# Kernel tuning notes

Hardware: AMD Instinct MI355X
Metric: run time of the kernel (lower is better)

Reference implementation:

```python
import jax, jax.numpy as jnp
import numpy as np

B, PTS, D = 8, 4096, 256          # batch, points per sample, hidden_size
QT, QR, QO = 3000, 216, 1         # num_queries: pos bins, 72*3 euler bins, openness


def setup_inputs() -> dict:
    key = jax.random.key(0)
    ks = jax.random.split(key, 11)
    N = B * PTS
    w = lambda k, s: jax.random.normal(k, s, jnp.float32) * 0.02
    return {
        "feat": jax.random.normal(ks[0], (N, D), jnp.float32),
        "npoints_in_batch": jnp.full((B,), PTS, jnp.int32),
        "queries_t": w(ks[1], (QT, D)),
        "Wk_t": w(ks[2], (D, D)),
        "Wv_t": w(ks[3], (D, D)),
        "queries_r": w(ks[4], (QR, D)),
        "Wk_r": w(ks[5], (D, D)),
        "Wv_r": w(ks[6], (D, D)),
        "queries_o": w(ks[7], (QO, D)),
        "Wk_o": w(ks[8], (D, D)),
        "Wv_o": w(ks[9], (D, D)),
    }


def _aggregate(feat, seg, queries, Wk, Wv):
    """Ragged cross-attention pooling + sum over feature dim.

    feat: (N, D) all points; seg: (N,) sample id per point.
    Equivalent to, per sample b: sum_d( softmax_n(q K_b^T/sqrt(D)) V_b )[q, d]
    => (B, Q) since sum over d commutes: attn @ V.sum(-1).
    """
    d = feat.shape[-1]
    k = feat @ Wk                                  # (N, D)
    vsum = (feat @ Wv).sum(-1)                     # (N,)  row-sum of values
    scores = (k @ queries.T) / jnp.sqrt(jnp.float32(d))  # (N, Q)
    m = jax.ops.segment_max(scores, seg, num_segments=B)  # (B, Q)
    e = jnp.exp(scores - m[seg])                   # (N, Q)
    denom = jax.ops.segment_sum(e, seg, num_segments=B)   # (B, Q)
    numer = jax.ops.segment_sum(e * vsum[:, None], seg, num_segments=B)
    return numer / denom                           # (B, Q)


def reference(feat, npoints_in_batch, queries_t, Wk_t, Wv_t,
              queries_r, Wk_r, Wv_r, queries_o, Wk_o, Wv_o):
    N = feat.shape[0]
    seg = jnp.repeat(jnp.arange(B, dtype=jnp.int32), npoints_in_batch,
                     total_repeat_length=N)
    xt = _aggregate(feat, seg, queries_t, Wk_t, Wv_t)  # (B, 3000)
    xr = _aggregate(feat, seg, queries_r, Wk_r, Wv_r)  # (B, 216)
    xo = _aggregate(feat, seg, queries_o, Wk_o, Wv_o)  # (B, 1)
    return (xt, xr, xo)
```

## Files before the change

kernel.cpp:

```cpp
#include <hip/hip_runtime.h>

typedef __attribute__((ext_vector_type(8))) short short8;
typedef __attribute__((ext_vector_type(4))) float f32x4;
typedef unsigned int u32;

#define D_ 256
#define QT_V 3000
#define QR_V 216
#define QO_V 1
#define QPT 3008
#define QPR 224
#define QPO 96
#define QPTOT 3328
#define WQ_TILES 104
#define NSPLIT 8
#define VPAD 32
#define SCALE 0.09016844005556021f
#define TILE_US 8192
#define PSTRIDE 264

__device__ __forceinline__ unsigned short f2bf(float f) {
    union { float f; unsigned int i; } u; u.f = f;
    unsigned int i = u.i + 0x7fffu + ((u.i >> 16) & 1u);
    return (unsigned short)(i >> 16);
}

__device__ __forceinline__ void async_cp16(const unsigned short* g, unsigned short* l) {
    __builtin_amdgcn_global_load_lds((const __attribute__((address_space(1))) u32*)g,
                                     (__attribute__((address_space(3))) u32*)l, 16, 0, 0);
}

__global__ __launch_bounds__(256) void prep_small(
    const float* __restrict__ wk_t, const float* __restrict__ wk_r,
    const float* __restrict__ wk_o,
    const float* __restrict__ wv_t, const float* __restrict__ wv_r,
    const float* __restrict__ wv_o,
    unsigned short* __restrict__ Wkb,
    float* __restrict__ wvsum, float* __restrict__ vsum, int N)
{
    int blk = blockIdx.x, tid = (int)threadIdx.x;
    if (blk < 3) {
        const float* Wk = (blk == 0) ? wk_t : ((blk == 1) ? wk_r : wk_o);
        const float* Wv = (blk == 0) ? wv_t : ((blk == 1) ? wv_r : wv_o);
        for (int i = tid; i < 16384; i += 256) {
            float4 v = ((const float4*)Wk)[i];
            ushort4 o;
            o.x = f2bf(v.x); o.y = f2bf(v.y); o.z = f2bf(v.z); o.w = f2bf(v.w);
            ((ushort4*)(Wkb + (size_t)blk * 65536))[i] = o;
        }
        const float* row = Wv + (size_t)tid * D_;
        float s = 0.f;
        for (int d = 0; d < D_; d += 4) {
            float4 v = *(const float4*)(row + d);
            s += v.x + v.y + v.z + v.w;
        }
        wvsum[blk * 256 + tid] = s;
    } else {
        if (tid < 3 * VPAD) {
            int h = tid / VPAD, i = tid % VPAD;
            vsum[(size_t)h * (N + VPAD) + N + i] = 0.f;
        }
    }
}

__global__ __launch_bounds__(256) void prep_mid(
    const float* __restrict__ feat,
    const float* __restrict__ wvsum,
    const float* __restrict__ q_t, const float* __restrict__ q_r,
    const float* __restrict__ q_o,
    const unsigned short* __restrict__ Wkb,
    unsigned short* __restrict__ featb,
    float* __restrict__ vsum,
    unsigned short* __restrict__ WqT,
    int N, int ntiles)
{
    __shared__ __align__(16) unsigned short lds[32 * PSTRIDE];
    int blk = blockIdx.x, tid = (int)threadIdx.x;
    int srow = tid >> 3, c8 = tid & 7;
    int wave = tid >> 6, lane = tid & 63;
    int col16 = lane & 15, quad = lane >> 4;

    if (blk < ntiles) {
        int t = blk;
        int row = t * 32 + srow;
        bool valid = row < N;
        float p0 = 0.f, p1 = 0.f, p2 = 0.f;
#pragma unroll
        for (int i = 0; i < 8; ++i) {
            int col = i * 32 + c8 * 4;
            float4 v;
            if (valid) v = *(const float4*)(feat + (size_t)row * D_ + col);
            else { v.x = v.y = v.z = v.w = 0.f; }
            ushort4 o;
            o.x = f2bf(v.x); o.y = f2bf(v.y); o.z = f2bf(v.z); o.w = f2bf(v.w);
            *(ushort4*)(lds + srow * PSTRIDE + col) = o;
            float4 w0 = *(const float4*)(wvsum + col);
            float4 w1 = *(const float4*)(wvsum + 256 + col);
            float4 w2 = *(const float4*)(wvsum + 512 + col);
            p0 += v.x * w0.x + v.y * w0.y + v.z * w0.z + v.w * w0.w;
            p1 += v.x * w1.x + v.y * w1.y + v.z * w1.z + v.w * w1.w;
            p2 += v.x * w2.x + v.y * w2.y + v.z * w2.z + v.w * w2.w;
        }
        p0 += __shfl_xor(p0, 1); p0 += __shfl_xor(p0, 2); p0 += __shfl_xor(p0, 4);
        p1 += __shfl_xor(p1, 1); p1 += __shfl_xor(p1, 2); p1 += __shfl_xor(p1, 4);
        p2 += __shfl_xor(p2, 1); p2 += __shfl_xor(p2, 2); p2 += __shfl_xor(p2, 4);
        if (c8 == 0 && valid) {
            vsum[0 * (size_t)(N + VPAD) + row] = p0;
            vsum[1 * (size_t)(N + VPAD) + row] = p1;
            vsum[2 * (size_t)(N + VPAD) + row] = p2;
        }
        __syncthreads();
#pragma unroll
        for (int i = 0; i < 4; ++i) {
            int cmb = wave * 4 + i;
            int kk = cmb >> 1, sub = cmb & 1;
            short8 v = *(const short8*)(lds + (sub * 16 + col16) * PSTRIDE
                                        + quad * 8 + kk * 32);
            *(short8*)(featb + (size_t)t * TILE_US + cmb * 512 + lane * 8) = v;
        }
    } else {
        int wq = blk - ntiles;
        const float* Q; int nvalid, lq0, outrow, h;
        if (wq < 94)       { Q = q_t; nvalid = QT_V; lq0 = wq * 32;         outrow = lq0;             h = 0; }
        else if (wq < 101) { Q = q_r; nvalid = QR_V; lq0 = (wq - 94) * 32;  outrow = QPT + lq0;       h = 1; }
        else               { Q = q_o; nvalid = QO_V; lq0 = (wq - 101) * 32; outrow = QPT + QPR + lq0; h = 2; }
        int row = lq0 + srow;
        bool valid = row < nvalid;
#pragma unroll
        for (int i = 0; i < 8; ++i) {
            int col = i * 32 + c8 * 4;
            float4 v;
            if (valid) v = *(const float4*)(Q + (size_t)row * D_ + col);
            else { v.x = v.y = v.z = v.w = 0.f; }
            ushort4 o;
            o.x = f2bf(v.x); o.y = f2bf(v.y); o.z = f2bf(v.z); o.w = f2bf(v.w);
            *(ushort4*)(lds + srow * PSTRIDE + col) = o;
        }
        __syncthreads();
        int c0 = wave * 64;
        f32x4 acc[2][4];
#pragma unroll
        for (int mt = 0; mt < 2; ++mt)
#pragma unroll
            for (int nt = 0; nt < 4; ++nt)
                acc[mt][nt] = f32x4{0.f, 0.f, 0.f, 0.f};
        const unsigned short* Wh = Wkb + (size_t)h * 65536;
#pragma unroll
        for (int kk = 0; kk < 8; ++kk) {
            short8 a0 = *(const short8*)(lds + col16 * PSTRIDE + quad * 8 + kk * 32);
            short8 a1 = *(const short8*)(lds + (16 + col16) * PSTRIDE + quad * 8 + kk * 32);
#pragma unroll
            for (int nt = 0; nt < 4; ++nt) {
                short8 bf = *(const short8*)(Wh + (size_t)(c0 + nt * 16 + col16) * D_
                                             + quad * 8 + kk * 32);
                acc[0][nt] = __builtin_amdgcn_mfma_f32_16x16x32_bf16(a0, bf, acc[0][nt], 0, 0, 0);
                acc[1][nt] = __builtin_amdgcn_mfma_f32_16x16x32_bf16(a1, bf, acc[1][nt], 0, 0, 0);
            }
        }
#pragma unroll
        for (int mt = 0; mt < 2; ++mt)
#pragma unroll
            for (int nt = 0; nt < 4; ++nt)
#pragma unroll
                for (int r = 0; r < 4; ++r) {
                    int orow = outrow + mt * 16 + quad * 4 + r;
                    int ocol = c0 + nt * 16 + col16;
                    WqT[(size_t)orow * D_ + ocol] = f2bf(acc[mt][nt][r] * SCALE);
                }
    }
}

__global__ __launch_bounds__(256, 4) void attn_main(
    const unsigned short* __restrict__ featb,
    const int* __restrict__ npts,
    const unsigned short* __restrict__ WqT,
    const float* __restrict__ vsum,
    float* __restrict__ partials, int N)
{
    __shared__ __align__(16) unsigned short lds[2][TILE_US];
    int b = blockIdx.z, qblock = blockIdx.y, chunk = blockIdx.x;
    int tid = (int)threadIdx.x;
    int wave = tid >> 6, lane = tid & 63;
    int col = lane & 15, quad = lane >> 4;

    int qp0 = qblock * 128 + wave * 32;
    int h = (qp0 < QPT) ? 0 : ((qp0 < QPT + QPR) ? 1 : 2);
    const float* vs = vsum + (size_t)h * (N + VPAD);

    int start = 0;
#pragma unroll 1
    for (int i = 0; i < b; ++i) start += npts[i];
    int end = start + npts[b];
    if (end > N) end = N;
    if (start < 0) start = 0;
    if (start > end) start = end;
    int bt0 = start >> 5, bt1 = (end + 31) >> 5;
    int ntc = (bt1 - bt0 + NSPLIT - 1) / NSPLIT;
    int ta = bt0 + chunk * ntc;
    int tb = ta + ntc; if (tb > bt1) tb = bt1;

    short8 bfrag[2][8];
#pragma unroll
    for (int qt = 0; qt < 2; ++qt) {
        const unsigned short* wr = WqT + (size_t)(qp0 + qt * 16 + col) * D_ + quad * 8;
#pragma unroll
        for (int kk = 0; kk < 8; ++kk)
            bfrag[qt][kk] = *(const short8*)(wr + kk * 32);
    }

    float den0 = 0.f, num0 = 0.f, den1 = 0.f, num1 = 0.f;
    int p = 0;
    if (ta < tb) {
        const unsigned short* g = featb + (size_t)ta * TILE_US + (wave * 4) * 512 + lane * 8;
#pragma unroll
        for (int i = 0; i < 4; ++i)
            async_cp16(g + i * 512, &lds[0][(wave * 4 + i) * 512]);
    }
#pragma unroll 1
    for (int t = ta; t < tb; ++t) {
        __syncthreads();
        if (t + 1 < tb) {
            const unsigned short* g = featb + (size_t)(t + 1) * TILE_US + (wave * 4) * 512 + lane * 8;
#pragma unroll
            for (int i = 0; i < 4; ++i)
                async_cp16(g + i * 512, &lds[p ^ 1][(wave * 4 + i) * 512]);
        }
        const unsigned short* lp = lds[p];
        f32x4 acc00 = {0.f,0.f,0.f,0.f}, acc01 = {0.f,0.f,0.f,0.f};
        f32x4 acc10 = {0.f,0.f,0.f,0.f}, acc11 = {0.f,0.f,0.f,0.f};
#pragma unroll
        for (int kk = 0; kk < 8; ++kk) {
            short8 a0 = *(const short8*)(lp + (kk * 2 + 0) * 512 + lane * 8);
            short8 a1 = *(const short8*)(lp + (kk * 2 + 1) * 512 + lane * 8);
            acc00 = __builtin_amdgcn_mfma_f32_16x16x32_bf16(a0, bfrag[0][kk], acc00, 0, 0, 0);
            acc10 = __builtin_amdgcn_mfma_f32_16x16x32_bf16(a0, bfrag[1][kk], acc10, 0, 0, 0);
            acc01 = __builtin_amdgcn_mfma_f32_16x16x32_bf16(a1, bfrag[0][kk], acc01, 0, 0, 0);
            acc11 = __builtin_amdgcn_mfma_f32_16x16x32_bf16(a1, bfrag[1][kk], acc11, 0, 0, 0);
        }
        int rb = t * 32 + quad * 4;
        f32x4 v0 = *(const f32x4*)(vs + rb);
        f32x4 v1 = *(const f32x4*)(vs + rb + 16);
        int r0 = t * 32;
        if (r0 >= start && r0 + 32 <= end) {
#pragma unroll
            for (int r = 0; r < 4; ++r) {
                float e00 = __builtin_amdgcn_exp2f(acc00[r]);
                float e01 = __builtin_amdgcn_exp2f(acc01[r]);
                float e10 = __builtin_amdgcn_exp2f(acc10[r]);
                float e11 = __builtin_amdgcn_exp2f(acc11[r]);
                den0 += e00 + e01; num0 += e00 * v0[r] + e01 * v1[r];
                den1 += e10 + e11; num1 += e10 * v0[r] + e11 * v1[r];
            }
        } else {
#pragma unroll
            for (int r = 0; r < 4; ++r) {
                int ra = rb + r, rb2 = rb + 16 + r;
                bool ma = (ra >= start) && (ra < end);
                bool mb = (rb2 >= start) && (rb2 < end);
                float e00 = ma ? __builtin_amdgcn_exp2f(acc00[r]) : 0.f;
                float e01 = mb ? __builtin_amdgcn_exp2f(acc01[r]) : 0.f;
                float e10 = ma ? __builtin_amdgcn_exp2f(acc10[r]) : 0.f;
                float e11 = mb ? __builtin_amdgcn_exp2f(acc11[r]) : 0.f;
                den0 += e00 + e01; num0 += e00 * v0[r] + e01 * v1[r];
                den1 += e10 + e11; num1 += e10 * v0[r] + e11 * v1[r];
            }
        }
        p ^= 1;
    }

    den0 += __shfl_xor(den0, 16); den0 += __shfl_xor(den0, 32);
    num0 += __shfl_xor(num0, 16); num0 += __shfl_xor(num0, 32);
    den1 += __shfl_xor(den1, 16); den1 += __shfl_xor(den1, 32);
    num1 += __shfl_xor(num1, 16); num1 += __shfl_xor(num1, 32);

    if (quad == 0) {
        size_t base = ((size_t)b * QPTOT + (qp0 + col)) * NSPLIT + chunk;
        partials[base * 2]     = den0;
        partials[base * 2 + 1] = num0;
        size_t base1 = base + (size_t)16 * NSPLIT;
        partials[base1 * 2]     = den1;
        partials[base1 * 2 + 1] = num1;
    }
}

__global__ __launch_bounds__(256) void combine_k(
    const float* __restrict__ partials,
    float* __restrict__ out, int Bn)
{
    int gid = blockIdx.x * 256 + threadIdx.x;
    int total = Bn * QPTOT;
    if (gid >= total) return;
    int b = gid / QPTOT, qp = gid - b * QPTOT;
    const float* p = partials + (size_t)gid * NSPLIT * 2;
    float den = 0.f, num = 0.f;
#pragma unroll
    for (int c = 0; c < NSPLIT; ++c) { den += p[c * 2]; num += p[c * 2 + 1]; }
    float val = (den > 0.f) ? (num / den) : 0.f;
    int oidx = -1;
    if (qp < QPT) {
        if (qp < QT_V) oidx = b * QT_V + qp;
    } else if (qp < QPT + QPR) {
        int q = qp - QPT;
        if (q < QR_V) oidx = Bn * QT_V + b * QR_V + q;
    } else {
        int q = qp - QPT - QPR;
        if (q < QO_V) oidx = Bn * (QT_V + QR_V) + b;
    }
    if (oidx >= 0) out[oidx] = val;
}

extern "C" void kernel_launch(void* const* d_in, const int* in_sizes, int n_in,
                              void* d_out, int out_size, void* d_ws, size_t ws_size,
                              hipStream_t stream)
{
    const float* feat = (const float*)d_in[0];
    const int* npts   = (const int*)d_in[1];
    const float* q_t  = (const float*)d_in[2];
    const float* wk_t = (const float*)d_in[3];
    const float* wv_t = (const float*)d_in[4];
    const float* q_r  = (const float*)d_in[5];
    const float* wk_r = (const float*)d_in[6];
    const float* wv_r = (const float*)d_in[7];
    const float* q_o  = (const float*)d_in[8];
    const float* wk_o = (const float*)d_in[9];
    const float* wv_o = (const float*)d_in[10];

    int N  = in_sizes[0] / D_;
    int Bn = in_sizes[1];
    int ntiles = (N + 31) / 32;

    char* ws = (char*)d_ws;
    size_t off = 0;
    unsigned short* WqT = (unsigned short*)(ws + off);
    off += (size_t)QPTOT * D_ * sizeof(unsigned short);
    off = (off + 255) & ~(size_t)255;
    unsigned short* featb = (unsigned short*)(ws + off);
    off += (size_t)ntiles * TILE_US * sizeof(unsigned short);
    off = (off + 255) & ~(size_t)255;
    unsigned short* Wkb = (unsigned short*)(ws + off);
    off += (size_t)3 * 65536 * sizeof(unsigned short);
    off = (off + 255) & ~(size_t)255;
    float* wvsum = (float*)(ws + off);
    off += 3 * D_ * sizeof(float);
    off = (off + 255) & ~(size_t)255;
    float* vsum = (float*)(ws + off);
    off += (size_t)3 * (N + VPAD) * sizeof(float);
    off = (off + 255) & ~(size_t)255;
    float* partials = (float*)(ws + off);
    off += (size_t)Bn * QPTOT * NSPLIT * 2 * sizeof(float);
    (void)ws_size;

    prep_small<<<4, 256, 0, stream>>>(wk_t, wk_r, wk_o, wv_t, wv_r, wv_o,
                                      Wkb, wvsum, vsum, N);
    prep_mid<<<ntiles + WQ_TILES, 256, 0, stream>>>(feat, wvsum, q_t, q_r, q_o,
                                                    Wkb, featb, vsum, WqT, N, ntiles);

    dim3 grid(NSPLIT, QPTOT / 128, Bn);
    attn_main<<<grid, 256, 0, stream>>>(featb, npts, WqT, vsum, partials, N);

    int total = Bn * QPTOT;
    combine_k<<<(total + 255) / 256, 256, 0, stream>>>(partials, (float*)d_out, Bn);
}
```

Before: 189.8 us.

## Load feature tiles directly from global into registers instead of LDS double-buffer

Removes the LDS double-buffered async global-to-LDS pipeline and the per-tile block barrier in attn_main. Each wave now loads its MFMA A-fragments for a tile straight from global memory into registers and then issues the MFMAs. The change also splits the softmax accumulators into independent per-fragment partial sums and lowers the launch-bounds occupancy hint from 4 to 3 blocks per CU to allow more registers. The aim is to drop barrier and LDS overhead. In exchange, every wave in a block re-reads the same tile from global memory or cache, and load latency is no longer hidden by explicit prefetching.

```diff
diff --git a/kernel.cpp b/kernel.cpp
--- a/kernel.cpp
+++ b/kernel.cpp
@@ -25,11 +25,6 @@
     return (unsigned short)(i >> 16);
 }
 
-__device__ __forceinline__ void async_cp16(const unsigned short* g, unsigned short* l) {
-    __builtin_amdgcn_global_load_lds((const __attribute__((address_space(1))) u32*)g,
-                                     (__attribute__((address_space(3))) u32*)l, 16, 0, 0);
-}
-
 __global__ __launch_bounds__(256) void prep_small(
     const float* __restrict__ wk_t, const float* __restrict__ wk_r,
     const float* __restrict__ wk_o,
@@ -170,14 +165,13 @@
     }
 }
 
-__global__ __launch_bounds__(256, 4) void attn_main(
+__global__ __launch_bounds__(256, 3) void attn_main(
     const unsigned short* __restrict__ featb,
     const int* __restrict__ npts,
     const unsigned short* __restrict__ WqT,
     const float* __restrict__ vsum,
     float* __restrict__ partials, int N)
 {
-    __shared__ __align__(16) unsigned short lds[2][TILE_US];
     int b = blockIdx.z, qblock = blockIdx.y, chunk = blockIdx.x;
     int tid = (int)threadIdx.x;
     int wave = tid >> 6, lane = tid & 63;
@@ -208,38 +202,31 @@
             bfrag[qt][kk] = *(const short8*)(wr + kk * 32);
     }
 
-    float den0 = 0.f, num0 = 0.f, den1 = 0.f, num1 = 0.f;
-    int p = 0;
-    if (ta < tb) {
-        const unsigned short* g = featb + (size_t)ta * TILE_US + (wave * 4) * 512 + lane * 8;
-#pragma unroll
-        for (int i = 0; i < 4; ++i)
-            async_cp16(g + i * 512, &lds[0][(wave * 4 + i) * 512]);
-    }
+    float den00 = 0.f, den01 = 0.f, den10 = 0.f, den11 = 0.f;
+    float num00 = 0.f, num01 = 0.f, num10 = 0.f, num11 = 0.f;
+
 #pragma unroll 1
     for (int t = ta; t < tb; ++t) {
-        __syncthreads();
-        if (t + 1 < tb) {
-            const unsigned short* g = featb + (size_t)(t + 1) * TILE_US + (wave * 4) * 512 + lane * 8;
-#pragma unroll
-            for (int i = 0; i < 4; ++i)
-                async_cp16(g + i * 512, &lds[p ^ 1][(wave * 4 + i) * 512]);
-        }
-        const unsigned short* lp = lds[p];
-        f32x4 acc00 = {0.f,0.f,0.f,0.f}, acc01 = {0.f,0.f,0.f,0.f};
-        f32x4 acc10 = {0.f,0.f,0.f,0.f}, acc11 = {0.f,0.f,0.f,0.f};
-#pragma unroll
-        for (int kk = 0; kk < 8; ++kk) {
-            short8 a0 = *(const short8*)(lp + (kk * 2 + 0) * 512 + lane * 8);
-            short8 a1 = *(const short8*)(lp + (kk * 2 + 1) * 512 + lane * 8);
-            acc00 = __builtin_amdgcn_mfma_f32_16x16x32_bf16(a0, bfrag[0][kk], acc00, 0, 0, 0);
-            acc10 = __builtin_amdgcn_mfma_f32_16x16x32_bf16(a0, bfrag[1][kk], acc10, 0, 0, 0);
-            acc01 = __builtin_amdgcn_mfma_f32_16x16x32_bf16(a1, bfrag[0][kk], acc01, 0, 0, 0);
-            acc11 = __builtin_amdgcn_mfma_f32_16x16x32_bf16(a1, bfrag[1][kk], acc11, 0, 0, 0);
-        }
+        const unsigned short* tp = featb + (size_t)t * TILE_US + lane * 8;
         int rb = t * 32 + quad * 4;
         f32x4 v0 = *(const f32x4*)(vs + rb);
         f32x4 v1 = *(const f32x4*)(vs + rb + 16);
+
+        short8 a0[8], a1[8];
+#pragma unroll
+        for (int kk = 0; kk < 8; ++kk) {
+            a0[kk] = *(const short8*)(tp + (kk * 2 + 0) * 512);
+            a1[kk] = *(const short8*)(tp + (kk * 2 + 1) * 512);
+        }
+        f32x4 acc00 = {0.f,0.f,0.f,0.f}, acc01 = {0.f,0.f,0.f,0.f};
+        f32x4 acc10 = {0.f,0.f,0.f,0.f}, acc11 = {0.f,0.f,0.f,0.f};
+#pragma unroll
+        for (int kk = 0; kk < 8; ++kk) {
+            acc00 = __builtin_amdgcn_mfma_f32_16x16x32_bf16(a0[kk], bfrag[0][kk], acc00, 0, 0, 0);
+            acc10 = __builtin_amdgcn_mfma_f32_16x16x32_bf16(a0[kk], bfrag[1][kk], acc10, 0, 0, 0);
+            acc01 = __builtin_amdgcn_mfma_f32_16x16x32_bf16(a1[kk], bfrag[0][kk], acc01, 0, 0, 0);
+            acc11 = __builtin_amdgcn_mfma_f32_16x16x32_bf16(a1[kk], bfrag[1][kk], acc11, 0, 0, 0);
+        }
         int r0 = t * 32;
         if (r0 >= start && r0 + 32 <= end) {
 #pragma unroll
@@ -248,8 +235,10 @@
                 float e01 = __builtin_amdgcn_exp2f(acc01[r]);
                 float e10 = __builtin_amdgcn_exp2f(acc10[r]);
                 float e11 = __builtin_amdgcn_exp2f(acc11[r]);
-                den0 += e00 + e01; num0 += e00 * v0[r] + e01 * v1[r];
-                den1 += e10 + e11; num1 += e10 * v0[r] + e11 * v1[r];
+                den00 += e00; num00 += e00 * v0[r];
+                den01 += e01; num01 += e01 * v1[r];
+                den10 += e10; num10 += e10 * v0[r];
+                den11 += e11; num11 += e11 * v1[r];
             }
         } else {
 #pragma unroll
@@ -261,13 +250,16 @@
                 float e01 = mb ? __builtin_amdgcn_exp2f(acc01[r]) : 0.f;
                 float e10 = ma ? __builtin_amdgcn_exp2f(acc10[r]) : 0.f;
                 float e11 = mb ? __builtin_amdgcn_exp2f(acc11[r]) : 0.f;
-                den0 += e00 + e01; num0 += e00 * v0[r] + e01 * v1[r];
-                den1 += e10 + e11; num1 += e10 * v0[r] + e11 * v1[r];
+                den00 += e00; num00 += e00 * v0[r];
+                den01 += e01; num01 += e01 * v1[r];
+                den10 += e10; num10 += e10 * v0[r];
+                den11 += e11; num11 += e11 * v1[r];
             }
         }
-        p ^= 1;
-    }
-
+    }
+
+    float den0 = den00 + den01, num0 = num00 + num01;
+    float den1 = den10 + den11, num1 = num10 + num11;
     den0 += __shfl_xor(den0, 16); den0 += __shfl_xor(den0, 32);
     num0 += __shfl_xor(num0, 16); num0 += __shfl_xor(num0, 32);
     den1 += __shfl_xor(den1, 16); den1 += __shfl_xor(den1, 32);
```

New measurement: 230.6 us. 1.22x slower.

## Merge prep kernels into one launch and raise split count of attention

Applied to the files above, without the earlier changes.

Folds the small weight-prep kernel into a single prep launch. The Wk bf16 conversion now happens inline, with fp32 weights read directly inside the WqT MFMA loop. Wv row-sums and the vsum projection move into a separate set of blocks that each recompute the Wv sums. This removes one kernel launch and a serial dependency. NSPLIT doubles from 8 to 16 to give the attention kernel more blocks across the point dimension, at the cost of more partials for the combine step to reduce.

```diff
diff --git a/kernel.cpp b/kernel.cpp
--- a/kernel.cpp
+++ b/kernel.cpp
@@ -13,7 +13,7 @@
 #define QPO 96
 #define QPTOT 3328
 #define WQ_TILES 104
-#define NSPLIT 8
+#define NSPLIT 16
 #define VPAD 32
 #define SCALE 0.09016844005556021f
 #define TILE_US 8192
@@ -30,49 +30,18 @@
                                      (__attribute__((address_space(3))) u32*)l, 16, 0, 0);
 }
 
-__global__ __launch_bounds__(256) void prep_small(
+__global__ __launch_bounds__(256) void prep(
+    const float* __restrict__ feat,
+    const float* __restrict__ q_t, const float* __restrict__ q_r,
+    const float* __restrict__ q_o,
     const float* __restrict__ wk_t, const float* __restrict__ wk_r,
     const float* __restrict__ wk_o,
     const float* __restrict__ wv_t, const float* __restrict__ wv_r,
     const float* __restrict__ wv_o,
-    unsigned short* __restrict__ Wkb,
-    float* __restrict__ wvsum, float* __restrict__ vsum, int N)
-{
-    int blk = blockIdx.x, tid = (int)threadIdx.x;
-    if (blk < 3) {
-        const float* Wk = (blk == 0) ? wk_t : ((blk == 1) ? wk_r : wk_o);
-        const float* Wv = (blk == 0) ? wv_t : ((blk == 1) ? wv_r : wv_o);
-        for (int i = tid; i < 16384; i += 256) {
-            float4 v = ((const float4*)Wk)[i];
-            ushort4 o;
-            o.x = f2bf(v.x); o.y = f2bf(v.y); o.z = f2bf(v.z); o.w = f2bf(v.w);
-            ((ushort4*)(Wkb + (size_t)blk * 65536))[i] = o;
-        }
-        const float* row = Wv + (size_t)tid * D_;
-        float s = 0.f;
-        for (int d = 0; d < D_; d += 4) {
-            float4 v = *(const float4*)(row + d);
-            s += v.x + v.y + v.z + v.w;
-        }
-        wvsum[blk * 256 + tid] = s;
-    } else {
-        if (tid < 3 * VPAD) {
-            int h = tid / VPAD, i = tid % VPAD;
-            vsum[(size_t)h * (N + VPAD) + N + i] = 0.f;
-        }
-    }
-}
-
-__global__ __launch_bounds__(256) void prep_mid(
-    const float* __restrict__ feat,
-    const float* __restrict__ wvsum,
-    const float* __restrict__ q_t, const float* __restrict__ q_r,
-    const float* __restrict__ q_o,
-    const unsigned short* __restrict__ Wkb,
     unsigned short* __restrict__ featb,
+    unsigned short* __restrict__ WqT,
     float* __restrict__ vsum,
-    unsigned short* __restrict__ WqT,
-    int N, int ntiles)
+    int N, int ntiles, int nvs)
 {
     __shared__ __align__(16) unsigned short lds[32 * PSTRIDE];
     int blk = blockIdx.x, tid = (int)threadIdx.x;
@@ -84,7 +53,6 @@
         int t = blk;
         int row = t * 32 + srow;
         bool valid = row < N;
-        float p0 = 0.f, p1 = 0.f, p2 = 0.f;
 #pragma unroll
         for (int i = 0; i < 8; ++i) {
             int col = i * 32 + c8 * 4;
@@ -94,20 +62,6 @@
             ushort4 o;
             o.x = f2bf(v.x); o.y = f2bf(v.y); o.z = f2bf(v.z); o.w = f2bf(v.w);
             *(ushort4*)(lds + srow * PSTRIDE + col) = o;
-            float4 w0 = *(const float4*)(wvsum + col);
-            float4 w1 = *(const float4*)(wvsum + 256 + col);
-            float4 w2 = *(const float4*)(wvsum + 512 + col);
-            p0 += v.x * w0.x + v.y * w0.y + v.z * w0.z + v.w * w0.w;
-            p1 += v.x * w1.x + v.y * w1.y + v.z * w1.z + v.w * w1.w;
-            p2 += v.x * w2.x + v.y * w2.y + v.z * w2.z + v.w * w2.w;
-        }
-        p0 += __shfl_xor(p0, 1); p0 += __shfl_xor(p0, 2); p0 += __shfl_xor(p0, 4);
-        p1 += __shfl_xor(p1, 1); p1 += __shfl_xor(p1, 2); p1 += __shfl_xor(p1, 4);
-        p2 += __shfl_xor(p2, 1); p2 += __shfl_xor(p2, 2); p2 += __shfl_xor(p2, 4);
-        if (c8 == 0 && valid) {
-            vsum[0 * (size_t)(N + VPAD) + row] = p0;
-            vsum[1 * (size_t)(N + VPAD) + row] = p1;
-            vsum[2 * (size_t)(N + VPAD) + row] = p2;
         }
         __syncthreads();
 #pragma unroll
@@ -118,12 +72,12 @@
                                         + quad * 8 + kk * 32);
             *(short8*)(featb + (size_t)t * TILE_US + cmb * 512 + lane * 8) = v;
         }
-    } else {
+    } else if (blk < ntiles + WQ_TILES) {
         int wq = blk - ntiles;
-        const float* Q; int nvalid, lq0, outrow, h;
-        if (wq < 94)       { Q = q_t; nvalid = QT_V; lq0 = wq * 32;         outrow = lq0;             h = 0; }
-        else if (wq < 101) { Q = q_r; nvalid = QR_V; lq0 = (wq - 94) * 32;  outrow = QPT + lq0;       h = 1; }
-        else               { Q = q_o; nvalid = QO_V; lq0 = (wq - 101) * 32; outrow = QPT + QPR + lq0; h = 2; }
+        const float* Q; const float* Wh; int nvalid, lq0, outrow;
+        if (wq < 94)       { Q = q_t; Wh = wk_t; nvalid = QT_V; lq0 = wq * 32;         outrow = lq0; }
+        else if (wq < 101) { Q = q_r; Wh = wk_r; nvalid = QR_V; lq0 = (wq - 94) * 32;  outrow = QPT + lq0; }
+        else               { Q = q_o; Wh = wk_o; nvalid = QO_V; lq0 = (wq - 101) * 32; outrow = QPT + QPR + lq0; }
         int row = lq0 + srow;
         bool valid = row < nvalid;
 #pragma unroll
@@ -144,15 +98,20 @@
 #pragma unroll
             for (int nt = 0; nt < 4; ++nt)
                 acc[mt][nt] = f32x4{0.f, 0.f, 0.f, 0.f};
-        const unsigned short* Wh = Wkb + (size_t)h * 65536;
 #pragma unroll
         for (int kk = 0; kk < 8; ++kk) {
             short8 a0 = *(const short8*)(lds + col16 * PSTRIDE + quad * 8 + kk * 32);
             short8 a1 = *(const short8*)(lds + (16 + col16) * PSTRIDE + quad * 8 + kk * 32);
 #pragma unroll
             for (int nt = 0; nt < 4; ++nt) {
-                short8 bf = *(const short8*)(Wh + (size_t)(c0 + nt * 16 + col16) * D_
-                                             + quad * 8 + kk * 32);
+                const float* wr = Wh + (size_t)(c0 + nt * 16 + col16) * D_ + quad * 8 + kk * 32;
+                float4 x = *(const float4*)(wr);
+                float4 y = *(const float4*)(wr + 4);
+                short8 bf;
+                bf[0] = (short)f2bf(x.x); bf[1] = (short)f2bf(x.y);
+                bf[2] = (short)f2bf(x.z); bf[3] = (short)f2bf(x.w);
+                bf[4] = (short)f2bf(y.x); bf[5] = (short)f2bf(y.y);
+                bf[6] = (short)f2bf(y.z); bf[7] = (short)f2bf(y.w);
                 acc[0][nt] = __builtin_amdgcn_mfma_f32_16x16x32_bf16(a0, bf, acc[0][nt], 0, 0, 0);
                 acc[1][nt] = __builtin_amdgcn_mfma_f32_16x16x32_bf16(a1, bf, acc[1][nt], 0, 0, 0);
             }
@@ -167,6 +126,54 @@
                     int ocol = c0 + nt * 16 + col16;
                     WqT[(size_t)orow * D_ + ocol] = f2bf(acc[mt][nt][r] * SCALE);
                 }
+    } else {
+        int v = blk - ntiles - WQ_TILES;
+        float* wv = (float*)lds;
+        for (int f0 = wave * 4; f0 < 768; f0 += 16) {
+            int f = f0 + (lane >> 4);
+            int hh = f >> 8, c = f & 255;
+            const float* base = ((hh == 0) ? wv_t : (hh == 1) ? wv_r : wv_o)
+                                + (size_t)c * D_;
+            float s = 0.f;
+#pragma unroll
+            for (int p = 0; p < 4; ++p) {
+                float4 x = *(const float4*)(base + p * 64 + (lane & 15) * 4);
+                s += x.x + x.y + x.z + x.w;
+            }
+            s += __shfl_xor(s, 1); s += __shfl_xor(s, 2);
+            s += __shfl_xor(s, 4); s += __shfl_xor(s, 8);
+            if ((lane & 15) == 0) wv[f] = s;
+        }
+        __syncthreads();
+        int r0 = v * 128;
+#pragma unroll 1
+        for (int pass = 0; pass < 32; ++pass) {
+            int row = r0 + pass * 4 + wave;
+            if (row < N) {
+                float4 fv = *(const float4*)(feat + (size_t)row * D_ + lane * 4);
+                float4 w0 = *(const float4*)(wv + lane * 4);
+                float4 w1 = *(const float4*)(wv + 256 + lane * 4);
+                float4 w2 = *(const float4*)(wv + 512 + lane * 4);
+                float p0 = fv.x * w0.x + fv.y * w0.y + fv.z * w0.z + fv.w * w0.w;
+                float p1 = fv.x * w1.x + fv.y * w1.y + fv.z * w1.z + fv.w * w1.w;
+                float p2 = fv.x * w2.x + fv.y * w2.y + fv.z * w2.z + fv.w * w2.w;
+#pragma unroll
+                for (int off = 32; off >= 1; off >>= 1) {
+                    p0 += __shfl_xor(p0, off);
+                    p1 += __shfl_xor(p1, off);
+                    p2 += __shfl_xor(p2, off);
+                }
+                if (lane == 0) {
+                    vsum[0 * (size_t)(N + VPAD) + row] = p0;
+                    vsum[1 * (size_t)(N + VPAD) + row] = p1;
+                    vsum[2 * (size_t)(N + VPAD) + row] = p2;
+                }
+            }
+        }
+        if (v == nvs - 1 && tid < 3 * VPAD) {
+            int hh = tid / VPAD, i = tid % VPAD;
+            vsum[(size_t)hh * (N + VPAD) + N + i] = 0.f;
+        }
     }
 }
 
@@ -328,6 +335,7 @@
     int N  = in_sizes[0] / D_;
     int Bn = in_sizes[1];
     int ntiles = (N + 31) / 32;
+    int nvs = (N + 127) / 128;
 
     char* ws = (char*)d_ws;
     size_t off = 0;
@@ -337,12 +345,6 @@
     unsigned short* featb = (unsigned short*)(ws + off);
     off += (size_t)ntiles * TILE_US * sizeof(unsigned short);
     off = (off + 255) & ~(size_t)255;
-    unsigned short* Wkb = (unsigned short*)(ws + off);
-    off += (size_t)3 * 65536 * sizeof(unsigned short);
-    off = (off + 255) & ~(size_t)255;
-    float* wvsum = (float*)(ws + off);
-    off += 3 * D_ * sizeof(float);
-    off = (off + 255) & ~(size_t)255;
     float* vsum = (float*)(ws + off);
     off += (size_t)3 * (N + VPAD) * sizeof(float);
     off = (off + 255) & ~(size_t)255;
@@ -350,10 +352,9 @@
     off += (size_t)Bn * QPTOT * NSPLIT * 2 * sizeof(float);
     (void)ws_size;
 
-    prep_small<<<4, 256, 0, stream>>>(wk_t, wk_r, wk_o, wv_t, wv_r, wv_o,
-                                      Wkb, wvsum, vsum, N);
-    prep_mid<<<ntiles + WQ_TILES, 256, 0, stream>>>(feat, wvsum, q_t, q_r, q_o,
-                                                    Wkb, featb, vsum, WqT, N, ntiles);
+    prep<<<ntiles + WQ_TILES + nvs, 256, 0, stream>>>(
+        feat, q_t, q_r, q_o, wk_t, wk_r, wk_o, wv_t, wv_r, wv_o,
+        featb, WqT, vsum, N, ntiles, nvs);
 
     dim3 grid(NSPLIT, QPTOT / 128, Bn);
     attn_main<<<grid, 256, 0, stream>>>(featb, npts, WqT, vsum, partials, N);
```

Result: slower. 208.7 us (+10.0%).

## Double per-wave query tile in attention and convert Wk inline

Applied to the files above, without the earlier changes.

Each wave in the main attention kernel now covers 64 query columns instead of 32, and each block covers 256 queries, so every LDS feature tile feeds twice as many MFMAs. Launch bounds are relaxed from 4 to 2 blocks per CU to leave room for the extra register fragments, and the query padding layout is rebalanced (rotation 256, openness 64) so blocks divide evenly. The Wk bf16 conversion pass is removed: the query-projection blocks read fp32 Wk directly and convert in registers, and the Wv row-sum is computed with coalesced wave-level reductions. The trade-off is higher register pressure and lower occupancy in exchange for more data reuse and one less prep pass.

```diff
diff --git a/kernel.cpp b/kernel.cpp
--- a/kernel.cpp
+++ b/kernel.cpp
@@ -9,9 +9,10 @@
 #define QR_V 216
 #define QO_V 1
 #define QPT 3008
-#define QPR 224
-#define QPO 96
+#define QPR2 256
+#define QPO2 64
 #define QPTOT 3328
+#define NQB 13
 #define WQ_TILES 104
 #define NSPLIT 8
 #define VPAD 32
@@ -30,35 +31,32 @@
                                      (__attribute__((address_space(3))) u32*)l, 16, 0, 0);
 }
 
-__global__ __launch_bounds__(256) void prep_small(
-    const float* __restrict__ wk_t, const float* __restrict__ wk_r,
-    const float* __restrict__ wk_o,
+__global__ __launch_bounds__(256) void prep_w(
     const float* __restrict__ wv_t, const float* __restrict__ wv_r,
     const float* __restrict__ wv_o,
-    unsigned short* __restrict__ Wkb,
     float* __restrict__ wvsum, float* __restrict__ vsum, int N)
 {
     int blk = blockIdx.x, tid = (int)threadIdx.x;
+    int wave = tid >> 6, lane = tid & 63;
     if (blk < 3) {
-        const float* Wk = (blk == 0) ? wk_t : ((blk == 1) ? wk_r : wk_o);
         const float* Wv = (blk == 0) ? wv_t : ((blk == 1) ? wv_r : wv_o);
-        for (int i = tid; i < 16384; i += 256) {
-            float4 v = ((const float4*)Wk)[i];
-            ushort4 o;
-            o.x = f2bf(v.x); o.y = f2bf(v.y); o.z = f2bf(v.z); o.w = f2bf(v.w);
-            ((ushort4*)(Wkb + (size_t)blk * 65536))[i] = o;
-        }
-        const float* row = Wv + (size_t)tid * D_;
-        float s = 0.f;
-        for (int d = 0; d < D_; d += 4) {
-            float4 v = *(const float4*)(row + d);
-            s += v.x + v.y + v.z + v.w;
-        }
-        wvsum[blk * 256 + tid] = s;
+        for (int f0 = wave * 4; f0 < 256; f0 += 16) {
+            int f = f0 + (lane >> 4);
+            const float* base = Wv + (size_t)f * D_;
+            float s = 0.f;
+#pragma unroll
+            for (int p = 0; p < 4; ++p) {
+                float4 x = *(const float4*)(base + p * 64 + (lane & 15) * 4);
+                s += x.x + x.y + x.z + x.w;
+            }
+            s += __shfl_xor(s, 1); s += __shfl_xor(s, 2);
+            s += __shfl_xor(s, 4); s += __shfl_xor(s, 8);
+            if ((lane & 15) == 0) wvsum[blk * 256 + f] = s;
+        }
     } else {
         if (tid < 3 * VPAD) {
-            int h = tid / VPAD, i = tid % VPAD;
-            vsum[(size_t)h * (N + VPAD) + N + i] = 0.f;
+            int hh = tid / VPAD, i = tid % VPAD;
+            vsum[(size_t)hh * (N + VPAD) + N + i] = 0.f;
         }
     }
 }
@@ -68,7 +66,8 @@
     const float* __restrict__ wvsum,
     const float* __restrict__ q_t, const float* __restrict__ q_r,
     const float* __restrict__ q_o,
-    const unsigned short* __restrict__ Wkb,
+    const float* __restrict__ wk_t, const float* __restrict__ wk_r,
+    const float* __restrict__ wk_o,
     unsigned short* __restrict__ featb,
     float* __restrict__ vsum,
     unsigned short* __restrict__ WqT,
@@ -120,10 +119,10 @@
         }
     } else {
         int wq = blk - ntiles;
-        const float* Q; int nvalid, lq0, outrow, h;
-        if (wq < 94)       { Q = q_t; nvalid = QT_V; lq0 = wq * 32;         outrow = lq0;             h = 0; }
-        else if (wq < 101) { Q = q_r; nvalid = QR_V; lq0 = (wq - 94) * 32;  outrow = QPT + lq0;       h = 1; }
-        else               { Q = q_o; nvalid = QO_V; lq0 = (wq - 101) * 32; outrow = QPT + QPR + lq0; h = 2; }
+        const float* Q; const float* Wh; int nvalid, lq0, outrow;
+        if (wq < 94)       { Q = q_t; Wh = wk_t; nvalid = QT_V; lq0 = wq * 32;          outrow = lq0; }
+        else if (wq < 102) { Q = q_r; Wh = wk_r; nvalid = QR_V; lq0 = (wq - 94) * 32;   outrow = QPT + lq0; }
+        else               { Q = q_o; Wh = wk_o; nvalid = QO_V; lq0 = (wq - 102) * 32;  outrow = QPT + QPR2 + lq0; }
         int row = lq0 + srow;
         bool valid = row < nvalid;
 #pragma unroll
@@ -144,15 +143,20 @@
 #pragma unroll
             for (int nt = 0; nt < 4; ++nt)
                 acc[mt][nt] = f32x4{0.f, 0.f, 0.f, 0.f};
-        const unsigned short* Wh = Wkb + (size_t)h * 65536;
 #pragma unroll
         for (int kk = 0; kk < 8; ++kk) {
             short8 a0 = *(const short8*)(lds + col16 * PSTRIDE + quad * 8 + kk * 32);
             short8 a1 = *(const short8*)(lds + (16 + col16) * PSTRIDE + quad * 8 + kk * 32);
 #pragma unroll
             for (int nt = 0; nt < 4; ++nt) {
-                short8 bf = *(const short8*)(Wh + (size_t)(c0 + nt * 16 + col16) * D_
-                                             + quad * 8 + kk * 32);
+                const float* wr = Wh + (size_t)(c0 + nt * 16 + col16) * D_ + quad * 8 + kk * 32;
+                float4 x = *(const float4*)(wr);
+                float4 y = *(const float4*)(wr + 4);
+                short8 bf;
+                bf[0] = (short)f2bf(x.x); bf[1] = (short)f2bf(x.y);
+                bf[2] = (short)f2bf(x.z); bf[3] = (short)f2bf(x.w);
+                bf[4] = (short)f2bf(y.x); bf[5] = (short)f2bf(y.y);
+                bf[6] = (short)f2bf(y.z); bf[7] = (short)f2bf(y.w);
                 acc[0][nt] = __builtin_amdgcn_mfma_f32_16x16x32_bf16(a0, bf, acc[0][nt], 0, 0, 0);
                 acc[1][nt] = __builtin_amdgcn_mfma_f32_16x16x32_bf16(a1, bf, acc[1][nt], 0, 0, 0);
             }
@@ -170,7 +174,7 @@
     }
 }
 
-__global__ __launch_bounds__(256, 4) void attn_main(
+__global__ __launch_bounds__(256, 2) void attn_main(
     const unsigned short* __restrict__ featb,
     const int* __restrict__ npts,
     const unsigned short* __restrict__ WqT,
@@ -183,8 +187,8 @@
     int wave = tid >> 6, lane = tid & 63;
     int col = lane & 15, quad = lane >> 4;
 
-    int qp0 = qblock * 128 + wave * 32;
-    int h = (qp0 < QPT) ? 0 : ((qp0 < QPT + QPR) ? 1 : 2);
+    int qp0 = qblock * 256 + wave * 64;
+    int h = (qp0 < QPT) ? 0 : ((qp0 < QPT + QPR2) ? 1 : 2);
     const float* vs = vsum + (size_t)h * (N + VPAD);
 
     int start = 0;
@@ -199,16 +203,17 @@
     int ta = bt0 + chunk * ntc;
     int tb = ta + ntc; if (tb > bt1) tb = bt1;
 
-    short8 bfrag[2][8];
-#pragma unroll
-    for (int qt = 0; qt < 2; ++qt) {
+    short8 bfrag[4][8];
+#pragma unroll
+    for (int qt = 0; qt < 4; ++qt) {
         const unsigned short* wr = WqT + (size_t)(qp0 + qt * 16 + col) * D_ + quad * 8;
 #pragma unroll
         for (int kk = 0; kk < 8; ++kk)
             bfrag[qt][kk] = *(const short8*)(wr + kk * 32);
     }
 
-    float den0 = 0.f, num0 = 0.f, den1 = 0.f, num1 = 0.f;
+    float den[4] = {0.f, 0.f, 0.f, 0.f};
+    float num[4] = {0.f, 0.f, 0.f, 0.f};
     int p = 0;
     if (ta < tb) {
         const unsigned short* g = featb + (size_t)ta * TILE_US + (wave * 4) * 512 + lane * 8;
@@ -226,16 +231,21 @@
                 async_cp16(g + i * 512, &lds[p ^ 1][(wave * 4 + i) * 512]);
         }
         const unsigned short* lp = lds[p];
-        f32x4 acc00 = {0.f,0.f,0.f,0.f}, acc01 = {0.f,0.f,0.f,0.f};
-        f32x4 acc10 = {0.f,0.f,0.f,0.f}, acc11 = {0.f,0.f,0.f,0.f};
+        f32x4 acc0[4], acc1[4];
+#pragma unroll
+        for (int qt = 0; qt < 4; ++qt) {
+            acc0[qt] = f32x4{0.f,0.f,0.f,0.f};
+            acc1[qt] = f32x4{0.f,0.f,0.f,0.f};
+        }
 #pragma unroll
         for (int kk = 0; kk < 8; ++kk) {
             short8 a0 = *(const short8*)(lp + (kk * 2 + 0) * 512 + lane * 8);
             short8 a1 = *(const short8*)(lp + (kk * 2 + 1) * 512 + lane * 8);
-            acc00 = __builtin_amdgcn_mfma_f32_16x16x32_bf16(a0, bfrag[0][kk], acc00, 0, 0, 0);
-            acc10 = __builtin_amdgcn_mfma_f32_16x16x32_bf16(a0, bfrag[1][kk], acc10, 0, 0, 0);
-            acc01 = __builtin_amdgcn_mfma_f32_16x16x32_bf16(a1, bfrag[0][kk], acc01, 0, 0, 0);
-            acc11 = __builtin_amdgcn_mfma_f32_16x16x32_bf16(a1, bfrag[1][kk], acc11, 0, 0, 0);
+#pragma unroll
+            for (int qt = 0; qt < 4; ++qt) {
+                acc0[qt] = __builtin_amdgcn_mfma_f32_16x16x32_bf16(a0, bfrag[qt][kk], acc0[qt], 0, 0, 0);
+                acc1[qt] = __builtin_amdgcn_mfma_f32_16x16x32_bf16(a1, bfrag[qt][kk], acc1[qt], 0, 0, 0);
+            }
         }
         int rb = t * 32 + quad * 4;
         f32x4 v0 = *(const f32x4*)(vs + rb);
@@ -243,43 +253,45 @@
         int r0 = t * 32;
         if (r0 >= start && r0 + 32 <= end) {
 #pragma unroll
-            for (int r = 0; r < 4; ++r) {
-                float e00 = __builtin_amdgcn_exp2f(acc00[r]);
-                float e01 = __builtin_amdgcn_exp2f(acc01[r]);
-                float e10 = __builtin_amdgcn_exp2f(acc10[r]);
-                float e11 = __builtin_amdgcn_exp2f(acc11[r]);
-                den0 += e00 + e01; num0 += e00 * v0[r] + e01 * v1[r];
-                den1 += e10 + e11; num1 += e10 * v0[r] + e11 * v1[r];
-            }
+            for (int qt = 0; qt < 4; ++qt)
+#pragma unroll
+                for (int r = 0; r < 4; ++r) {
+                    float e0 = __builtin_amdgcn_exp2f(acc0[qt][r]);
+                    float e1 = __builtin_amdgcn_exp2f(acc1[qt][r]);
+                    den[qt] += e0 + e1;
+                    num[qt] += e0 * v0[r] + e1 * v1[r];
+                }
         } else {
 #pragma unroll
             for (int r = 0; r < 4; ++r) {
                 int ra = rb + r, rb2 = rb + 16 + r;
                 bool ma = (ra >= start) && (ra < end);
                 bool mb = (rb2 >= start) && (rb2 < end);
-                float e00 = ma ? __builtin_amdgcn_exp2f(acc00[r]) : 0.f;
-                float e01 = mb ? __builtin_amdgcn_exp2f(acc01[r]) : 0.f;
-                float e10 = ma ? __builtin_amdgcn_exp2f(acc10[r]) : 0.f;
-                float e11 = mb ? __builtin_amdgcn_exp2f(acc11[r]) : 0.f;
-                den0 += e00 + e01; num0 += e00 * v0[r] + e01 * v1[r];
-                den1 += e10 + e11; num1 += e10 * v0[r] + e11 * v1[r];
+#pragma unroll
+                for (int qt = 0; qt < 4; ++qt) {
+                    float e0 = ma ? __builtin_amdgcn_exp2f(acc0[qt][r]) : 0.f;
+                    float e1 = mb ? __builtin_amdgcn_exp2f(acc1[qt][r]) : 0.f;
+                    den[qt] += e0 + e1;
+                    num[qt] += e0 * v0[r] + e1 * v1[r];
+                }
             }
         }
         p ^= 1;
     }
 
-    den0 += __shfl_xor(den0, 16); den0 += __shfl_xor(den0, 32);
-    num0 += __shfl_xor(num0, 16); num0 += __shfl_xor(num0, 32);
-    den1 += __shfl_xor(den1, 16); den1 += __shfl_xor(den1, 32);
-    num1 += __shfl_xor(num1, 16); num1 += __shfl_xor(num1, 32);
+#pragma unroll
+    for (int qt = 0; qt < 4; ++qt) {
+        den[qt] += __shfl_xor(den[qt], 16); den[qt] += __shfl_xor(den[qt], 32);
+        num[qt] += __shfl_xor(num[qt], 16); num[qt] += __shfl_xor(num[qt], 32);
+    }
 
     if (quad == 0) {
-        size_t base = ((size_t)b * QPTOT + (qp0 + col)) * NSPLIT + chunk;
-        partials[base * 2]     = den0;
-        partials[base * 2 + 1] = num0;
-        size_t base1 = base + (size_t)16 * NSPLIT;
-        partials[base1 * 2]     = den1;
-        partials[base1 * 2 + 1] = num1;
+#pragma unroll
+        for (int qt = 0; qt < 4; ++qt) {
+            size_t base = ((size_t)b * QPTOT + (qp0 + qt * 16 + col)) * NSPLIT + chunk;
+            partials[base * 2]     = den[qt];
+            partials[base * 2 + 1] = num[qt];
+        }
     }
 }
 
@@ -299,11 +311,11 @@
     int oidx = -1;
     if (qp < QPT) {
         if (qp < QT_V) oidx = b * QT_V + qp;
-    } else if (qp < QPT + QPR) {
+    } else if (qp < QPT + QPR2) {
         int q = qp - QPT;
         if (q < QR_V) oidx = Bn * QT_V + b * QR_V + q;
     } else {
-        int q = qp - QPT - QPR;
+        int q = qp - QPT - QPR2;
         if (q < QO_V) oidx = Bn * (QT_V + QR_V) + b;
     }
     if (oidx >= 0) out[oidx] = val;
@@ -337,9 +349,6 @@
     unsigned short* featb = (unsigned short*)(ws + off);
     off += (size_t)ntiles * TILE_US * sizeof(unsigned short);
     off = (off + 255) & ~(size_t)255;
-    unsigned short* Wkb = (unsigned short*)(ws + off);
-    off += (size_t)3 * 65536 * sizeof(unsigned short);
-    off = (off + 255) & ~(size_t)255;
     float* wvsum = (float*)(ws + off);
     off += 3 * D_ * sizeof(float);
     off = (off + 255) & ~(size_t)255;
@@ -350,12 +359,12 @@
     off += (size_t)Bn * QPTOT * NSPLIT * 2 * sizeof(float);
     (void)ws_size;
 
-    prep_small<<<4, 256, 0, stream>>>(wk_t, wk_r, wk_o, wv_t, wv_r, wv_o,
-                                      Wkb, wvsum, vsum, N);
-    prep_mid<<<ntiles + WQ_TILES, 256, 0, stream>>>(feat, wvsum, q_t, q_r, q_o,
-                                                    Wkb, featb, vsum, WqT, N, ntiles);
-
-    dim3 grid(NSPLIT, QPTOT / 128, Bn);
+    prep_w<<<4, 256, 0, stream>>>(wv_t, wv_r, wv_o, wvsum, vsum, N);
+    prep_mid<<<ntiles + WQ_TILES, 256, 0, stream>>>(
+        feat, wvsum, q_t, q_r, q_o, wk_t, wk_r, wk_o,
+        featb, vsum, WqT, N, ntiles);
+
+    dim3 grid(NSPLIT, NQB, Bn);
     attn_main<<<grid, 256, 0, stream>>>(featb, npts, WqT, vsum, partials, N);
 
     int total = Bn * QPTOT;
```

After: 181.8 us. 1.04x faster.
